# Optimization experiments

Hardware: AMD Instinct MI355X
Metric: run time of the kernel (lower is better)

Reference implementation:

```python
import jax, jax.numpy as jnp
import numpy as np

RES = (160, 160, 160)            # (X, Y, Z)
AABB_MIN, AABB_MAX = -1.3, 1.3
DEG = 2
SH_DIM = (DEG + 1) ** 2          # 9
N_SAMPLES = 480                  # 'plenoxels': mean(res)*3*voxel_mul
NEAR, FAR = 0.2, 6.0
WHITE_BKGD = True
N_RAYS = 2048

C0 = 0.28209479177387814
C1 = 0.4886025119029199
C2 = (1.0925484305920792, -1.0925484305920792, 0.31539156525252005,
      -1.0925484305920792, 0.5462742152960396)


def sh_encoder(dirs):
    # real spherical harmonics up to degree 2 of the normalized view dir
    d = dirs / jnp.linalg.norm(dirs, axis=-1, keepdims=True)
    x, y, z = d[..., 0], d[..., 1], d[..., 2]
    return jnp.stack([
        jnp.full_like(x, C0),
        -C1 * y, C1 * z, -C1 * x,
        C2[0] * x * y, C2[1] * y * z,
        C2[2] * (2.0 * z * z - x * x - y * y),
        C2[3] * x * z, C2[4] * (x * x - y * y),
    ], axis=-1)                                     # [..., 9]


def trilinear_sample(grid, coords):
    # grid: [C, X, Y, Z]; coords: [..., 3] in (-1, 1).
    # torch F.grid_sample convention: coord x indexes last dim (Z), y -> Y, z -> X.
    # align_corners=True, padding_mode='zeros'.
    Cc, X, Y, Z = grid.shape
    gf = grid.reshape(Cc, -1)
    fx = (coords[..., 0] + 1.0) * 0.5 * (Z - 1)
    fy = (coords[..., 1] + 1.0) * 0.5 * (Y - 1)
    fz = (coords[..., 2] + 1.0) * 0.5 * (X - 1)
    x0f = jnp.floor(fx); y0f = jnp.floor(fy); z0f = jnp.floor(fz)
    wx = fx - x0f; wy = fy - y0f; wz = fz - z0f
    x0 = x0f.astype(jnp.int32); y0 = y0f.astype(jnp.int32); z0 = z0f.astype(jnp.int32)
    out = jnp.zeros(coords.shape[:-1] + (Cc,), dtype=grid.dtype)
    for dz in (0, 1):
        for dy in (0, 1):
            for dx in (0, 1):
                ix = x0 + dx; iy = y0 + dy; iz = z0 + dz
                valid = ((ix >= 0) & (ix < Z) & (iy >= 0) & (iy < Y)
                         & (iz >= 0) & (iz < X))
                w = ((wx if dx else 1.0 - wx)
                     * (wy if dy else 1.0 - wy)
                     * (wz if dz else 1.0 - wz)) * valid
                lin = (jnp.clip(iz, 0, X - 1) * Y + jnp.clip(iy, 0, Y - 1)) * Z \
                      + jnp.clip(ix, 0, Z - 1)
                vals = jnp.take(gf, lin, axis=1)    # [C, ...]
                out = out + jnp.moveaxis(vals, 0, -1) * w[..., None]
    return out                                      # [..., C]


def get_intersections(rays_o, rays_d, aabb, step, n):
    off_pos = (aabb[1] - rays_o) / rays_d
    off_neg = (aabb[0] - rays_o) / rays_d
    start = jnp.max(jnp.minimum(off_pos, off_neg), axis=-1, keepdims=True)
    start = jnp.clip(start, NEAR, FAR)
    steps = jnp.arange(n, dtype=rays_o.dtype)[None, :]
    return start + steps * step                     # [N, n]


def setup_inputs() -> dict:
    key = jax.random.key(0)
    k1, k2, k3, k4 = jax.random.split(key, 4)
    rays_o = jax.random.normal(k1, (N_RAYS, 3), jnp.float32) * 0.1   # inside aabb
    rays_d = jax.random.normal(k2, (N_RAYS, 3), jnp.float32)
    sigma_data = 0.1 + 0.05 * jax.random.normal(k3, (1,) + RES, jnp.float32)
    rgb_data = 0.01 * jax.random.normal(k4, (3 * SH_DIM,) + RES, jnp.float32)
    return {"rays_o": rays_o, "rays_d": rays_d,
            "sigma_data": sigma_data, "rgb_data": rgb_data}


def reference(rays_o, rays_d, sigma_data, rgb_data):
    dt = rays_o.dtype
    aabb = jnp.array([[AABB_MIN] * 3, [AABB_MAX] * 3], dtype=dt)
    aabb_size = aabb[1] - aabb[0]
    inv_aabb_size = 2.0 / aabb_size
    step = jnp.linalg.norm(aabb_size) / N_SAMPLES   # voxel_len

    inter = jax.lax.stop_gradient(
        get_intersections(rays_o, rays_d, aabb, step, N_SAMPLES))  # [N,S]
    pts = rays_o[:, None, :] + rays_d[:, None, :] * inter[:, :-1, None]  # [N,S-1,3]
    pn = (pts - aabb[0]) * inv_aabb_size - 1.0       # normalized (-1,1)

    sigma = jax.nn.relu(trilinear_sample(sigma_data, pn)[..., 0])   # [N,S-1]

    dists = jnp.diff(inter, axis=1) * jnp.linalg.norm(rays_d, axis=-1, keepdims=True)
    alpha = 1.0 - jnp.exp(-sigma * dists)
    cum_light = jnp.concatenate(
        [jnp.ones((alpha.shape[0], 1), dtype=dt),
         jnp.cumprod(1.0 - alpha[:, :-1] + 1e-10, axis=-1)], axis=-1)
    abs_light = alpha * cum_light                    # [N,S-1]

    sh_mult = sh_encoder(rays_d)                     # [N,9]
    rgb_feat = trilinear_sample(rgb_data, pn)        # [N,S-1,27]
    rgb_feat = rgb_feat.reshape(rgb_feat.shape[0], rgb_feat.shape[1], 3, SH_DIM)
    sh_rgb = jnp.einsum('nsck,nk->nsc', rgb_feat, sh_mult)

    rgb = jax.nn.sigmoid(sh_rgb)
    rgb_map = jnp.einsum('ns,nsc->nc', abs_light, rgb)
    if WHITE_BKGD:
        rgb_map = rgb_map + (1.0 - abs_light.sum(-1, keepdims=True))
    return rgb_map
```

## Files before the change

### kernel.cpp

```cpp
#include <hip/hip_runtime.h>
#include <math.h>

#define RESN  160
#define VOX   4096000
#define YSTR  160
#define ZSTR  25600
#define NPTS  478
#define NRAYS 2048

typedef float f2_u __attribute__((ext_vector_type(2), aligned(4)));

__device__ __forceinline__ float plane_interior(const float* __restrict__ p,
                                                float w00, float w01, float w10, float w11,
                                                float wx0, float wx1)
{
    f2_u a = *(const f2_u*)(p);
    f2_u b = *(const f2_u*)(p + YSTR);
    f2_u c = *(const f2_u*)(p + ZSTR);
    f2_u d = *(const f2_u*)(p + ZSTR + YSTR);
    float v0 = fmaf(a.y, wx1, a.x * wx0);
    float v1 = fmaf(b.y, wx1, b.x * wx0);
    float v2 = fmaf(c.y, wx1, c.x * wx0);
    float v3 = fmaf(d.y, wx1, d.x * wx0);
    return fmaf(v3, w11, fmaf(v2, w10, fmaf(v1, w01, v0 * w00)));
}

__global__ __launch_bounds__(64)
void plenoxel_render(const float* __restrict__ rays_o,
                     const float* __restrict__ rays_d,
                     const float* __restrict__ sig,
                     const float* __restrict__ rgb,
                     float* __restrict__ out)
{
    const int ray  = blockIdx.x;
    const int lane = threadIdx.x;

    const float ox = rays_o[ray*3+0], oy = rays_o[ray*3+1], oz = rays_o[ray*3+2];
    const float dxr = rays_d[ray*3+0], dyr = rays_d[ray*3+1], dzr = rays_d[ray*3+2];

    const float h = 2.6f * 1.7320508075688772f / 480.0f;

    const float ax = (1.3f - ox) / dxr, bx = (-1.3f - ox) / dxr;
    const float ay = (1.3f - oy) / dyr, by = (-1.3f - oy) / dyr;
    const float az = (1.3f - oz) / dzr, bz = (-1.3f - oz) / dzr;
    float start = fmaxf(fmaxf(fminf(ax, bx), fminf(ay, by)), fminf(az, bz));
    start = fminf(fmaxf(start, 0.2f), 6.0f);

    const float B = 1.3164f;
    const float mx1 = ( B - ox) / dxr, mx0 = (-B - ox) / dxr;
    const float my1 = ( B - oy) / dyr, my0 = (-B - oy) / dyr;
    const float mz1 = ( B - oz) / dzr, mz0 = (-B - oz) / dzr;
    float tl = fmaxf(fmaxf(fminf(mx0, mx1), fminf(my0, my1)), fminf(mz0, mz1));
    float th = fminf(fminf(fmaxf(mx0, mx1), fmaxf(my0, my1)), fmaxf(mz0, mz1));
    tl = fmaxf(tl, start);
    th = fminf(th, fmaf((float)NPTS, h, start));
    int s_lo, s_hi;
    if (th < tl) { s_lo = 0; s_hi = -1; }
    else {
        s_lo = max(0,    (int)floorf((tl - start) / h) - 1);
        s_hi = min(NPTS, (int)ceilf ((th - start) / h) + 1);
    }

    const float dsq  = dxr*dxr + dyr*dyr + dzr*dzr;
    const float dinv = rsqrtf(dsq);
    const float dn   = sqrtf(dsq);
    const float X = dxr * dinv, Y = dyr * dinv, Z = dzr * dinv;
    const float shv[9] = {
        0.28209479177387814f,
        -0.4886025119029199f * Y,
         0.4886025119029199f * Z,
        -0.4886025119029199f * X,
         1.0925484305920792f * X * Y,
        -1.0925484305920792f * Y * Z,
         0.31539156525252005f * (2.0f * Z * Z - X * X - Y * Y),
        -1.0925484305920792f * X * Z,
         0.5462742152960396f * (X * X - Y * Y),
    };
    const float dist = h * dn;

    float accR = 0.f, accG = 0.f, accB = 0.f, accL = 0.f;
    float carry = 1.0f;

    for (int basei = s_lo; basei <= s_hi; basei += 64) {
        const int s = basei + lane;
        float alpha = 0.f, cr = 0.f, cg = 0.f, cb = 0.f;
        if (s <= s_hi) {
            const float t  = fmaf((float)s, h, start);
            const float px = fmaf(dxr, t, ox);
            const float py = fmaf(dyr, t, oy);
            const float pz = fmaf(dzr, t, oz);
            const float fx = fmaf(px, 61.153846153846f, 79.5f);
            const float fy = fmaf(py, 61.153846153846f, 79.5f);
            const float fz = fmaf(pz, 61.153846153846f, 79.5f);
            const float fxf = floorf(fx), fyf = floorf(fy), fzf = floorf(fz);
            const int   x0 = (int)fxf, y0 = (int)fyf, z0 = (int)fzf;
            const float wx1 = fx - fxf, wy1 = fy - fyf, wz1 = fz - fzf;
            const float wx0 = 1.f - wx1, wy0 = 1.f - wy1, wz0 = 1.f - wz1;

            float sv = 0.f, a0 = 0.f, a1 = 0.f, a2 = 0.f;

            if (x0 >= 0 && x0 <= 158 && y0 >= 0 && y0 <= 158 && z0 >= 0 && z0 <= 158) {
                const float w00 = wz0*wy0, w01 = wz0*wy1, w10 = wz1*wy0, w11 = wz1*wy1;
                const size_t bofs = (size_t)z0 * ZSTR + (size_t)y0 * YSTR + (size_t)x0;
                sv = plane_interior(sig + bofs, w00, w01, w10, w11, wx0, wx1);
                const float* rp = rgb + bofs;
                #pragma unroll
                for (int c = 0; c < 3; ++c) {
                    float sc = 0.f;
                    #pragma unroll
                    for (int k = 0; k < 9; ++k) {
                        const float v = plane_interior(rp + (size_t)(c*9+k)*VOX,
                                                       w00, w01, w10, w11, wx0, wx1);
                        sc = fmaf(v, shv[k], sc);
                    }
                    if (c == 0) a0 = sc; else if (c == 1) a1 = sc; else a2 = sc;
                }
            } else {
                const float vwx0 = (x0   >= 0 && x0   < RESN) ? wx0 : 0.f;
                const float vwx1 = (x0+1 >= 0 && x0+1 < RESN) ? wx1 : 0.f;
                const float vwy0 = (y0   >= 0 && y0   < RESN) ? wy0 : 0.f;
                const float vwy1 = (y0+1 >= 0 && y0+1 < RESN) ? wy1 : 0.f;
                const float vwz0 = (z0   >= 0 && z0   < RESN) ? wz0 : 0.f;
                const float vwz1 = (z0+1 >= 0 && z0+1 < RESN) ? wz1 : 0.f;
                const int cx0 = min(max(x0,   0), RESN-1), cx1 = min(max(x0+1, 0), RESN-1);
                const int cy0 = min(max(y0,   0), RESN-1), cy1 = min(max(y0+1, 0), RESN-1);
                const int cz0 = min(max(z0,   0), RESN-1), cz1 = min(max(z0+1, 0), RESN-1);
                const float cw[8] = { vwz0*vwy0*vwx0, vwz0*vwy0*vwx1,
                                      vwz0*vwy1*vwx0, vwz0*vwy1*vwx1,
                                      vwz1*vwy0*vwx0, vwz1*vwy0*vwx1,
                                      vwz1*vwy1*vwx0, vwz1*vwy1*vwx1 };
                const size_t co[8] = {
                    (size_t)cz0*ZSTR + (size_t)cy0*YSTR + cx0,
                    (size_t)cz0*ZSTR + (size_t)cy0*YSTR + cx1,
                    (size_t)cz0*ZSTR + (size_t)cy1*YSTR + cx0,
                    (size_t)cz0*ZSTR + (size_t)cy1*YSTR + cx1,
                    (size_t)cz1*ZSTR + (size_t)cy0*YSTR + cx0,
                    (size_t)cz1*ZSTR + (size_t)cy0*YSTR + cx1,
                    (size_t)cz1*ZSTR + (size_t)cy1*YSTR + cx0,
                    (size_t)cz1*ZSTR + (size_t)cy1*YSTR + cx1 };
                #pragma unroll
                for (int j = 0; j < 8; ++j) {
                    if (cw[j] != 0.f) {
                        const float wj = cw[j];
                        sv = fmaf(sig[co[j]], wj, sv);
                        const float* rp = rgb + co[j];
                        float t0 = 0.f, t1 = 0.f, t2 = 0.f;
                        #pragma unroll
                        for (int k = 0; k < 9; ++k) {
                            t0 = fmaf(rp[(size_t)(k     )*VOX], shv[k], t0);
                            t1 = fmaf(rp[(size_t)(k +  9)*VOX], shv[k], t1);
                            t2 = fmaf(rp[(size_t)(k + 18)*VOX], shv[k], t2);
                        }
                        a0 = fmaf(t0, wj, a0);
                        a1 = fmaf(t1, wj, a1);
                        a2 = fmaf(t2, wj, a2);
                    }
                }
            }

            sv = fmaxf(sv, 0.f);
            alpha = 1.f - __expf(-sv * dist);
            cr = __fdividef(1.f, 1.f + __expf(-a0));
            cg = __fdividef(1.f, 1.f + __expf(-a1));
            cb = __fdividef(1.f, 1.f + __expf(-a2));
        }

        float m = (s <= s_hi) ? (1.f - alpha + 1e-10f) : 1.f;
        float incl = m;
        #pragma unroll
        for (int off = 1; off < 64; off <<= 1) {
            float nb = __shfl_up(incl, off);
            if (lane >= off) incl *= nb;
        }
        float excl = __shfl_up(incl, 1);
        if (lane == 0) excl = 1.f;

        const float T = carry * excl;
        const float w = T * alpha;
        accR = fmaf(w, cr, accR);
        accG = fmaf(w, cg, accG);
        accB = fmaf(w, cb, accB);
        accL += w;
        carry *= __shfl(incl, 63);
    }

    #pragma unroll
    for (int off = 32; off; off >>= 1) {
        accR += __shfl_xor(accR, off);
        accG += __shfl_xor(accG, off);
        accB += __shfl_xor(accB, off);
        accL += __shfl_xor(accL, off);
    }
    if (lane == 0) {
        const float bg = 1.f - accL;
        out[ray*3+0] = accR + bg;
        out[ray*3+1] = accG + bg;
        out[ray*3+2] = accB + bg;
    }
}

extern "C" void kernel_launch(void* const* d_in, const int* in_sizes, int n_in,
                              void* d_out, int out_size, void* d_ws, size_t ws_size,
                              hipStream_t stream) {
    const float* rays_o = (const float*)d_in[0];
    const float* rays_d = (const float*)d_in[1];
    const float* sig    = (const float*)d_in[2];
    const float* rgb    = (const float*)d_in[3];
    float* out = (float*)d_out;
    plenoxel_render<<<NRAYS, 64, 0, stream>>>(rays_o, rays_d, sig, rgb, out);
}
```

Measured before the change: 645.8 us.

## Repack grid into interleaved bf16 voxel records and split rays across four waves

```diff
diff --git a/kernel.cpp b/kernel.cpp
--- a/kernel.cpp
+++ b/kernel.cpp
@@ -7,33 +7,48 @@
 #define ZSTR  25600
 #define NPTS  478
 #define NRAYS 2048
+#define REC   32
 
 typedef float f2_u __attribute__((ext_vector_type(2), aligned(4)));
 
-__device__ __forceinline__ float plane_interior(const float* __restrict__ p,
-                                                float w00, float w01, float w10, float w11,
-                                                float wx0, float wx1)
+__global__ __launch_bounds__(256)
+void transpose_grid(const float* __restrict__ sig, const float* __restrict__ rgb,
+                    unsigned short* __restrict__ rec)
 {
-    f2_u a = *(const f2_u*)(p);
-    f2_u b = *(const f2_u*)(p + YSTR);
-    f2_u c = *(const f2_u*)(p + ZSTR);
-    f2_u d = *(const f2_u*)(p + ZSTR + YSTR);
-    float v0 = fmaf(a.y, wx1, a.x * wx0);
-    float v1 = fmaf(b.y, wx1, b.x * wx0);
-    float v2 = fmaf(c.y, wx1, c.x * wx0);
-    float v3 = fmaf(d.y, wx1, d.x * wx0);
-    return fmaf(v3, w11, fmaf(v2, w10, fmaf(v1, w01, v0 * w00)));
-}
-
-__global__ __launch_bounds__(64)
-void plenoxel_render(const float* __restrict__ rays_o,
-                     const float* __restrict__ rays_d,
-                     const float* __restrict__ sig,
-                     const float* __restrict__ rgb,
-                     float* __restrict__ out)
+    const int v = blockIdx.x * 256 + threadIdx.x;
+    float vals[32];
+    vals[0] = sig[v];
+    #pragma unroll
+    for (int k = 0; k < 27; ++k) vals[1 + k] = rgb[(size_t)k * VOX + v];
+    vals[28] = vals[29] = vals[30] = vals[31] = 0.f;
+    unsigned short h[32];
+    #pragma unroll
+    for (int k = 0; k < 32; ++k) {
+        unsigned u = __float_as_uint(vals[k]);
+        unsigned r = (u + 0x7FFFu + ((u >> 16) & 1u)) >> 16;
+        h[k] = (unsigned short)r;
+    }
+    uint4* dst = (uint4*)(rec + (size_t)v * REC);
+    const uint4* src = (const uint4*)h;
+    #pragma unroll
+    for (int i = 0; i < 4; ++i) dst[i] = src[i];
+}
+
+__device__ __forceinline__ void bf2(unsigned u, float& lo, float& hi) {
+    lo = __uint_as_float(u << 16);
+    hi = __uint_as_float(u & 0xFFFF0000u);
+}
+
+__global__ __launch_bounds__(256)
+void plenoxel_render2(const float* __restrict__ rays_o,
+                      const float* __restrict__ rays_d,
+                      const unsigned short* __restrict__ rec,
+                      float* __restrict__ out)
 {
     const int ray  = blockIdx.x;
-    const int lane = threadIdx.x;
+    const int tid  = threadIdx.x;
+    const int wave = tid >> 6;
+    const int lane = tid & 63;
 
     const float ox = rays_o[ray*3+0], oy = rays_o[ray*3+1], oz = rays_o[ray*3+2];
     const float dxr = rays_d[ray*3+0], dyr = rays_d[ray*3+1], dzr = rays_d[ray*3+2];
@@ -81,6 +96,224 @@
     float accR = 0.f, accG = 0.f, accB = 0.f, accL = 0.f;
     float carry = 1.0f;
 
+    const int nlive = s_hi - s_lo + 1;
+    if (nlive > 0) {
+        const int chunk = (nlive + 3) >> 2;
+        const int my_lo = s_lo + wave * chunk;
+        const int my_hi = min(my_lo + chunk - 1, s_hi);
+
+        for (int basei = my_lo; basei <= my_hi; basei += 64) {
+            const int s = basei + lane;
+            float alpha = 0.f, cr = 0.f, cg = 0.f, cb = 0.f;
+            if (s <= my_hi) {
+                const float t  = fmaf((float)s, h, start);
+                const float px = fmaf(dxr, t, ox);
+                const float py = fmaf(dyr, t, oy);
+                const float pz = fmaf(dzr, t, oz);
+                const float fx = fmaf(px, 61.153846153846f, 79.5f);
+                const float fy = fmaf(py, 61.153846153846f, 79.5f);
+                const float fz = fmaf(pz, 61.153846153846f, 79.5f);
+                const float fxf = floorf(fx), fyf = floorf(fy), fzf = floorf(fz);
+                const int   x0 = (int)fxf, y0 = (int)fyf, z0 = (int)fzf;
+                const float wx1 = fx - fxf, wy1 = fy - fyf, wz1 = fz - fzf;
+                const float wx0 = 1.f - wx1, wy0 = 1.f - wy1, wz0 = 1.f - wz1;
+
+                float sv = 0.f, a0 = 0.f, a1 = 0.f, a2 = 0.f;
+
+                if (x0 >= 0 && x0 <= 158 && y0 >= 0 && y0 <= 158 && z0 >= 0 && z0 <= 158) {
+                    const float wzy[4] = { wz0*wy0, wz0*wy1, wz1*wy0, wz1*wy1 };
+                    const int   offp[4] = { 0, YSTR*REC, ZSTR*REC, (ZSTR+YSTR)*REC };
+                    const size_t base = ((size_t)z0 * ZSTR + (size_t)y0 * YSTR + x0) * REC;
+                    #pragma unroll
+                    for (int p = 0; p < 4; ++p) {
+                        const uint4* P = (const uint4*)(rec + base + offp[p]);
+                        uint4 q0[4], q1[4];
+                        q0[0]=P[0]; q0[1]=P[1]; q0[2]=P[2]; q0[3]=P[3];
+                        q1[0]=P[4]; q1[1]=P[5]; q1[2]=P[6]; q1[3]=P[7];
+                        const float wA = wzy[p] * wx0, wB = wzy[p] * wx1;
+                        #pragma unroll
+                        for (int q = 0; q < 4; ++q) {
+                            const unsigned* u0 = (const unsigned*)&q0[q];
+                            const unsigned* u1 = (const unsigned*)&q1[q];
+                            #pragma unroll
+                            for (int d = 0; d < 4; ++d) {
+                                const int ch = q*8 + d*2;
+                                if (ch >= 28) break;
+                                float l0, h0, l1, h1;
+                                bf2(u0[d], l0, h0);
+                                bf2(u1[d], l1, h1);
+                                const float vA = fmaf(l1, wB, l0 * wA);
+                                const float vBv= fmaf(h1, wB, h0 * wA);
+                                if (ch == 0) sv += vA;
+                                else {
+                                    const int j = ch - 1;
+                                    const float c = shv[j % 9] * vA;
+                                    if (j < 9) a0 += c; else if (j < 18) a1 += c; else a2 += c;
+                                }
+                                if (ch + 1 < 28) {
+                                    const int j = ch;
+                                    const float c = shv[j % 9] * vBv;
+                                    if (j < 9) a0 += c; else if (j < 18) a1 += c; else a2 += c;
+                                }
+                            }
+                        }
+                    }
+                } else {
+                    const float vwx[2] = { (x0   >= 0 && x0   < RESN) ? wx0 : 0.f,
+                                           (x0+1 >= 0 && x0+1 < RESN) ? wx1 : 0.f };
+                    const float vwy[2] = { (y0   >= 0 && y0   < RESN) ? wy0 : 0.f,
+                                           (y0+1 >= 0 && y0+1 < RESN) ? wy1 : 0.f };
+                    const float vwz[2] = { (z0   >= 0 && z0   < RESN) ? wz0 : 0.f,
+                                           (z0+1 >= 0 && z0+1 < RESN) ? wz1 : 0.f };
+                    const int cx[2] = { min(max(x0,0),RESN-1), min(max(x0+1,0),RESN-1) };
+                    const int cy[2] = { min(max(y0,0),RESN-1), min(max(y0+1,0),RESN-1) };
+                    const int cz[2] = { min(max(z0,0),RESN-1), min(max(z0+1,0),RESN-1) };
+                    for (int dz = 0; dz < 2; ++dz)
+                    for (int dy = 0; dy < 2; ++dy)
+                    for (int dx = 0; dx < 2; ++dx) {
+                        const float w = vwz[dz]*vwy[dy]*vwx[dx];
+                        if (w == 0.f) continue;
+                        const uint4* P = (const uint4*)(rec +
+                            ((size_t)cz[dz]*ZSTR + (size_t)cy[dy]*YSTR + cx[dx]) * REC);
+                        uint4 qq[4]; qq[0]=P[0]; qq[1]=P[1]; qq[2]=P[2]; qq[3]=P[3];
+                        #pragma unroll
+                        for (int q = 0; q < 4; ++q) {
+                            const unsigned* u = (const unsigned*)&qq[q];
+                            #pragma unroll
+                            for (int d = 0; d < 4; ++d) {
+                                const int ch = q*8 + d*2;
+                                if (ch >= 28) break;
+                                float lo, hi; bf2(u[d], lo, hi);
+                                if (ch == 0) sv = fmaf(lo, w, sv);
+                                else {
+                                    const int j = ch - 1;
+                                    const float c = shv[j % 9] * lo * w;
+                                    if (j < 9) a0 += c; else if (j < 18) a1 += c; else a2 += c;
+                                }
+                                if (ch + 1 < 28) {
+                                    const int j = ch;
+                                    const float c = shv[j % 9] * hi * w;
+                                    if (j < 9) a0 += c; else if (j < 18) a1 += c; else a2 += c;
+                                }
+                            }
+                        }
+                    }
+                }
+
+                sv = fmaxf(sv, 0.f);
+                alpha = 1.f - __expf(-sv * dist);
+                cr = __fdividef(1.f, 1.f + __expf(-a0));
+                cg = __fdividef(1.f, 1.f + __expf(-a1));
+                cb = __fdividef(1.f, 1.f + __expf(-a2));
+            }
+
+            float m = (s <= my_hi) ? (1.f - alpha + 1e-10f) : 1.f;
+            float incl = m;
+            #pragma unroll
+            for (int off = 1; off < 64; off <<= 1) {
+                float nb = __shfl_up(incl, off);
+                if (lane >= off) incl *= nb;
+            }
+            float excl = __shfl_up(incl, 1);
+            if (lane == 0) excl = 1.f;
+
+            const float T = carry * excl;
+            const float w = T * alpha;
+            accR = fmaf(w, cr, accR);
+            accG = fmaf(w, cg, accG);
+            accB = fmaf(w, cb, accB);
+            accL += w;
+            carry *= __shfl(incl, 63);
+        }
+    }
+
+    #pragma unroll
+    for (int off = 32; off; off >>= 1) {
+        accR += __shfl_xor(accR, off);
+        accG += __shfl_xor(accG, off);
+        accB += __shfl_xor(accB, off);
+        accL += __shfl_xor(accL, off);
+    }
+
+    __shared__ float sP[4], sR[4], sG[4], sB[4], sL[4];
+    if (lane == 0) { sP[wave]=carry; sR[wave]=accR; sG[wave]=accG; sB[wave]=accB; sL[wave]=accL; }
+    __syncthreads();
+    if (tid == 0) {
+        float T = 1.f, R = 0.f, G = 0.f, Bc = 0.f, L = 0.f;
+        #pragma unroll
+        for (int w = 0; w < 4; ++w) {
+            R  += T * sR[w];
+            G  += T * sG[w];
+            Bc += T * sB[w];
+            L  += T * sL[w];
+            T  *= sP[w];
+        }
+        const float bg = 1.f - L;
+        out[ray*3+0] = R  + bg;
+        out[ray*3+1] = G  + bg;
+        out[ray*3+2] = Bc + bg;
+    }
+}
+
+__device__ __forceinline__ float plane_interior(const float* __restrict__ p,
+                                                float w00, float w01, float w10, float w11,
+                                                float wx0, float wx1)
+{
+    f2_u a = *(const f2_u*)(p);
+    f2_u b = *(const f2_u*)(p + YSTR);
+    f2_u c = *(const f2_u*)(p + ZSTR);
+    f2_u d = *(const f2_u*)(p + ZSTR + YSTR);
+    float v0 = fmaf(a.y, wx1, a.x * wx0);
+    float v1 = fmaf(b.y, wx1, b.x * wx0);
+    float v2 = fmaf(c.y, wx1, c.x * wx0);
+    float v3 = fmaf(d.y, wx1, d.x * wx0);
+    return fmaf(v3, w11, fmaf(v2, w10, fmaf(v1, w01, v0 * w00)));
+}
+
+__global__ __launch_bounds__(64)
+void plenoxel_render_f32(const float* __restrict__ rays_o,
+                         const float* __restrict__ rays_d,
+                         const float* __restrict__ sig,
+                         const float* __restrict__ rgb,
+                         float* __restrict__ out)
+{
+    const int ray  = blockIdx.x;
+    const int lane = threadIdx.x;
+    const float ox = rays_o[ray*3+0], oy = rays_o[ray*3+1], oz = rays_o[ray*3+2];
+    const float dxr = rays_d[ray*3+0], dyr = rays_d[ray*3+1], dzr = rays_d[ray*3+2];
+    const float h = 2.6f * 1.7320508075688772f / 480.0f;
+    const float ax = (1.3f - ox) / dxr, bx = (-1.3f - ox) / dxr;
+    const float ay = (1.3f - oy) / dyr, by = (-1.3f - oy) / dyr;
+    const float az = (1.3f - oz) / dzr, bz = (-1.3f - oz) / dzr;
+    float start = fmaxf(fmaxf(fminf(ax, bx), fminf(ay, by)), fminf(az, bz));
+    start = fminf(fmaxf(start, 0.2f), 6.0f);
+    const float B = 1.3164f;
+    const float mx1 = ( B - ox) / dxr, mx0 = (-B - ox) / dxr;
+    const float my1 = ( B - oy) / dyr, my0 = (-B - oy) / dyr;
+    const float mz1 = ( B - oz) / dzr, mz0 = (-B - oz) / dzr;
+    float tl = fmaxf(fmaxf(fminf(mx0, mx1), fminf(my0, my1)), fminf(mz0, mz1));
+    float th = fminf(fminf(fmaxf(mx0, mx1), fmaxf(my0, my1)), fmaxf(mz0, mz1));
+    tl = fmaxf(tl, start);
+    th = fminf(th, fmaf((float)NPTS, h, start));
+    int s_lo, s_hi;
+    if (th < tl) { s_lo = 0; s_hi = -1; }
+    else {
+        s_lo = max(0,    (int)floorf((tl - start) / h) - 1);
+        s_hi = min(NPTS, (int)ceilf ((th - start) / h) + 1);
+    }
+    const float dsq  = dxr*dxr + dyr*dyr + dzr*dzr;
+    const float dinv = rsqrtf(dsq);
+    const float dn   = sqrtf(dsq);
+    const float X = dxr * dinv, Y = dyr * dinv, Z = dzr * dinv;
+    const float shv[9] = {
+        0.28209479177387814f, -0.4886025119029199f * Y, 0.4886025119029199f * Z,
+        -0.4886025119029199f * X, 1.0925484305920792f * X * Y, -1.0925484305920792f * Y * Z,
+        0.31539156525252005f * (2.0f * Z * Z - X * X - Y * Y),
+        -1.0925484305920792f * X * Z, 0.5462742152960396f * (X * X - Y * Y),
+    };
+    const float dist = h * dn;
+    float accR = 0.f, accG = 0.f, accB = 0.f, accL = 0.f;
+    float carry = 1.0f;
     for (int basei = s_lo; basei <= s_hi; basei += 64) {
         const int s = basei + lane;
         float alpha = 0.f, cr = 0.f, cg = 0.f, cb = 0.f;
@@ -96,9 +329,7 @@
             const int   x0 = (int)fxf, y0 = (int)fyf, z0 = (int)fzf;
             const float wx1 = fx - fxf, wy1 = fy - fyf, wz1 = fz - fzf;
             const float wx0 = 1.f - wx1, wy0 = 1.f - wy1, wz0 = 1.f - wz1;
-
             float sv = 0.f, a0 = 0.f, a1 = 0.f, a2 = 0.f;
-
             if (x0 >= 0 && x0 <= 158 && y0 >= 0 && y0 <= 158 && z0 >= 0 && z0 <= 158) {
                 const float w00 = wz0*wy0, w01 = wz0*wy1, w10 = wz1*wy0, w11 = wz1*wy1;
                 const size_t bofs = (size_t)z0 * ZSTR + (size_t)y0 * YSTR + (size_t)x0;
@@ -157,14 +388,12 @@
                     }
                 }
             }
-
             sv = fmaxf(sv, 0.f);
             alpha = 1.f - __expf(-sv * dist);
             cr = __fdividef(1.f, 1.f + __expf(-a0));
             cg = __fdividef(1.f, 1.f + __expf(-a1));
             cb = __fdividef(1.f, 1.f + __expf(-a2));
         }
-
         float m = (s <= s_hi) ? (1.f - alpha + 1e-10f) : 1.f;
         float incl = m;
         #pragma unroll
@@ -174,7 +403,6 @@
         }
         float excl = __shfl_up(incl, 1);
         if (lane == 0) excl = 1.f;
-
         const float T = carry * excl;
         const float w = T * alpha;
         accR = fmaf(w, cr, accR);
@@ -183,7 +411,6 @@
         accL += w;
         carry *= __shfl(incl, 63);
     }
-
     #pragma unroll
     for (int off = 32; off; off >>= 1) {
         accR += __shfl_xor(accR, off);
@@ -207,5 +434,13 @@
     const float* sig    = (const float*)d_in[2];
     const float* rgb    = (const float*)d_in[3];
     float* out = (float*)d_out;
-    plenoxel_render<<<NRAYS, 64, 0, stream>>>(rays_o, rays_d, sig, rgb, out);
-}
+
+    const size_t need = (size_t)VOX * REC * sizeof(unsigned short);
+    if (ws_size >= need) {
+        unsigned short* rec = (unsigned short*)d_ws;
+        transpose_grid<<<VOX / 256, 256, 0, stream>>>(sig, rgb, rec);
+        plenoxel_render2<<<NRAYS, 256, 0, stream>>>(rays_o, rays_d, rec, out);
+    } else {
+        plenoxel_render_f32<<<NRAYS, 64, 0, stream>>>(rays_o, rays_d, sig, rgb, out);
+    }
+}
```

New measurement: 667.3 us. 1.03x slower.
